# Optimization experiments

Measured on AMD Instinct MI355X. Metric: run time of the kernel, lower is better.

## Reference

```python
import jax, jax.numpy as jnp
import numpy as np

B, L, C, H, W = 2, 4, 64, 80, 80
DISCRETE_RATIO, DOWNSAMPLE_RATE, NUM_ITER = 0.4, 2, 2


def _conv2d(x, w, b):
    y = jax.lax.conv_general_dilated(x, w, (1, 1), 'SAME',
                                     dimension_numbers=('NCHW', 'OIHW', 'NCHW'))
    return y + b[None, :, None, None]


def _get_transformation_matrix(M, h, w):
    # shift(center) @ [R 0; 0 1] @ shift(-center), then add raw translation (kornia-style)
    R = M[:, :2, :2]
    center = jnp.array([w / 2.0, h / 2.0], M.dtype)
    trans = center[None, :] - jnp.einsum('nij,j->ni', R, center) + M[:, :, 2]
    return jnp.concatenate([R, trans[:, :, None]], axis=2)  # (N,2,3)


def _warp_affine(src, M, mode):
    # src (N,C,h,w); M (N,2,3) maps src pixels -> dst pixels; sample src at M^{-1} @ dst
    # (equivalent to F.affine_grid/grid_sample with align_corners=True, zeros padding)
    N, Cc, h, w = src.shape
    bottom = jnp.tile(jnp.array([[[0.0, 0.0, 1.0]]], src.dtype), (N, 1, 1))
    Minv = jnp.linalg.inv(jnp.concatenate([M, bottom], axis=1))
    yy, xx = jnp.meshgrid(jnp.arange(h, dtype=src.dtype),
                          jnp.arange(w, dtype=src.dtype), indexing='ij')
    pts = jnp.stack([xx.ravel(), yy.ravel(), jnp.ones(h * w, src.dtype)], 0)  # (3,P)
    sp = jnp.einsum('nij,jp->nip', Minv, pts)
    sx, sy = sp[:, 0], sp[:, 1]  # (N,P) source pixel coords
    flat = src.reshape(N, Cc, h * w)

    def gather(ix, iy):
        valid = ((ix >= 0) & (ix < w) & (iy >= 0) & (iy < h)).astype(src.dtype)
        idx = jnp.clip(iy, 0, h - 1) * w + jnp.clip(ix, 0, w - 1)
        vals = jnp.take_along_axis(flat, jnp.broadcast_to(idx[:, None, :], (N, Cc, h * w)), axis=2)
        return vals * valid[:, None, :]

    if mode == 'nearest':
        out = gather(jnp.round(sx).astype(jnp.int32), jnp.round(sy).astype(jnp.int32))
    else:
        x0 = jnp.floor(sx); y0 = jnp.floor(sy)
        fx = (sx - x0)[:, None, :]; fy = (sy - y0)[:, None, :]
        x0 = x0.astype(jnp.int32); y0 = y0.astype(jnp.int32)
        out = (gather(x0, y0) * (1 - fx) * (1 - fy)
               + gather(x0 + 1, y0) * fx * (1 - fy)
               + gather(x0, y0 + 1) * (1 - fx) * fy
               + gather(x0 + 1, y0 + 1) * fx * fy)
    return out.reshape(N, Cc, h, w)


def _forward(x, pairwise_t_matrix, msg_w, msg_b, gates_w, gates_b, can_w, can_b, mlp_w, mlp_b):
    feats = x.reshape(B, L, C, H, W)
    # rows [0,1], cols [0,1,3] of the 4x4 SE(3) matrices; discretize translation
    t = pairwise_t_matrix[..., :2, :][..., jnp.array([0, 1, 3])]  # (B,L,L,2,3)
    t = t.at[..., 2].set(t[..., 2] / (DISCRETE_RATIO * DOWNSAMPLE_RATE))
    T = _get_transformation_matrix(t.reshape(-1, 2, 3), H, W)  # (B*L*L,2,3), flat index (b, j, i)
    mask = _warp_affine(jnp.ones((B * L * L, 1, H, W), x.dtype), T, 'nearest').reshape(B, L, L, 1, H, W)

    for _ in range(NUM_ITER):
        # 'b c h w -> b c w h' + flip(last): coordinate-convention fix (H==W)
        y = jnp.flip(jnp.swapaxes(feats, -1, -2), axis=-1)  # (B,L,C,H,W)
        # warp neighbor j into ego i frame with T[b,j,i]
        src = jnp.broadcast_to(y[:, :, None], (B, L, L, C, H, W)).reshape(-1, C, H, W)
        neighbor = _warp_affine(src, T, 'bilinear')
        ego = jnp.broadcast_to(y[:, None], (B, L, L, C, H, W)).reshape(-1, C, H, W)
        msg = _conv2d(jnp.concatenate([neighbor, ego], axis=1), msg_w, msg_b)
        msg = msg.reshape(B, L, L, C, H, W) * mask
        agg = msg.mean(axis=1)  # 'avg' over neighbors j -> (B,L,C,H,W)
        cat_feat = jnp.concatenate([y, agg], axis=2).reshape(B * L, 2 * C, H, W)
        # single ConvGRU step with zero initial hidden state
        h0 = jnp.zeros((B * L, C, H, W), x.dtype)
        gates = _conv2d(jnp.concatenate([cat_feat, h0], axis=1), gates_w, gates_b)
        reset = jax.nn.sigmoid(gates[:, :C])
        update = jax.nn.sigmoid(gates[:, C:])
        cand = jnp.tanh(_conv2d(jnp.concatenate([cat_feat, reset * h0], axis=1), can_w, can_b))
        h1 = (1.0 - update) * h0 + update * cand
        # undo the coordinate fix: flip(last) then 'c w h -> c h w'
        feats = jnp.swapaxes(jnp.flip(h1.reshape(B, L, C, H, W), axis=-1), -1, -2)

    out = feats[:, 0]  # ego agent of each sample, (B,C,H,W)
    return jnp.einsum('bchw,oc->bhwo', out, mlp_w) + mlp_b  # nn.Linear on channel-last


def setup_inputs() -> dict:
    key = jax.random.key(0)
    ks = jax.random.split(key, 12)
    x = jax.random.normal(ks[0], (B * L, C, H, W), dtype=jnp.float32)
    record_len = jnp.full((B,), L, dtype=jnp.int32)
    # realistic SE(2) pairwise transforms embedded in 4x4 homogeneous matrices
    ang = jax.random.uniform(ks[1], (B, L, L), minval=-0.3, maxval=0.3)
    tx = jax.random.uniform(ks[2], (B, L, L), minval=-8.0, maxval=8.0)
    ty = jax.random.uniform(ks[3], (B, L, L), minval=-8.0, maxval=8.0)
    c, s = jnp.cos(ang), jnp.sin(ang)
    z, o = jnp.zeros_like(ang), jnp.ones_like(ang)
    pairwise_t_matrix = jnp.stack([c, -s, z, tx,
                                   s, c, z, ty,
                                   z, z, o, z,
                                   z, z, z, o], axis=-1).reshape(B, L, L, 4, 4).astype(jnp.float32)
    prior_encoding = jax.random.normal(ks[4], (B * L, 3), dtype=jnp.float32)  # unused by forward
    sc = 0.05
    return {
        'x': x,
        'record_len': record_len,
        'pairwise_t_matrix': pairwise_t_matrix,
        'prior_encoding': prior_encoding,
        'msg_w': jax.random.normal(ks[5], (C, 2 * C, 3, 3), dtype=jnp.float32) * sc,
        'msg_b': jnp.zeros((C,), jnp.float32),
        'gates_w': jax.random.normal(ks[6], (2 * C, 3 * C, 3, 3), dtype=jnp.float32) * sc,
        'gates_b': jnp.zeros((2 * C,), jnp.float32),
        'can_w': jax.random.normal(ks[7], (C, 3 * C, 3, 3), dtype=jnp.float32) * sc,
        'can_b': jnp.zeros((C,), jnp.float32),
        'mlp_w': jax.random.normal(ks[8], (C, C), dtype=jnp.float32) * sc,
        'mlp_b': jnp.zeros((C,), jnp.float32),
    }


def reference(x, record_len, pairwise_t_matrix, prior_encoding,
              msg_w, msg_b, gates_w, gates_b, can_w, can_b, mlp_w, mlp_b):
    # record_len is fixed to L for every sample; prior_encoding is unused by the torch forward
    return _forward(x, pairwise_t_matrix, msg_w, msg_b, gates_w, gates_b,
                    can_w, can_b, mlp_w, mlp_b)
```

## Files before the change

kernel.cpp:

```cpp
#include <hip/hip_runtime.h>
#include <math.h>

#define WD 80
#define HW 6400
#define PW 82
#define PPX 6790
#define NIMG 8
#define NPAIR 32
#define RR 4
#define STG 960

typedef short bf16x8 __attribute__((ext_vector_type(8)));
typedef float f32x4 __attribute__((ext_vector_type(4)));

__device__ __forceinline__ float bf2f(unsigned short u) {
    return __uint_as_float(((unsigned)u) << 16);
}
__device__ __forceinline__ unsigned short f2bf(float f) {
    unsigned u = __float_as_uint(f);
    u += 0x7fff + ((u >> 16) & 1);
    return (unsigned short)(u >> 16);
}

__global__ void prep_mats(const float* __restrict__ P, float* __restrict__ mats) {
    int p = threadIdx.x;
    if (p >= NPAIR) return;
    const float* m = P + p * 16;
    float m00 = m[0], m01 = m[1], m02 = m[3] / 0.8f;
    float m10 = m[4], m11 = m[5], m12 = m[7] / 0.8f;
    float cx = 40.0f, cy = 40.0f;
    float tx = cx - (m00 * cx + m01 * cy) + m02;
    float ty = cy - (m10 * cx + m11 * cy) + m12;
    float det = m00 * m11 - m01 * m10;
    float id = 1.0f / det;
    float a00 =  m11 * id, a01 = -m01 * id;
    float a10 = -m10 * id, a11 =  m00 * id;
    float a02 = -(a00 * tx + a01 * ty);
    float a12 = -(a10 * tx + a11 * ty);
    float* o = mats + p * 6;
    o[0] = a00; o[1] = a01; o[2] = a02;
    o[3] = a10; o[4] = a11; o[5] = a12;
}

__global__ void make_mask(const float* __restrict__ mats, float* __restrict__ mask) {
    int p = blockIdx.x;
    const float* a = mats + p * 6;
    float a0 = a[0], a1 = a[1], a2 = a[2], a3 = a[3], a4 = a[4], a5 = a[5];
    for (int q = threadIdx.x; q < HW; q += blockDim.x) {
        float x = (float)(q % WD), y = (float)(q / WD);
        float sx = a0 * x + a1 * y + a2;
        float sy = a3 * x + a4 * y + a5;
        int ix = (int)rintf(sx), iy = (int)rintf(sy);
        mask[p * HW + q] = (ix >= 0 && ix < WD && iy >= 0 && iy < WD) ? 1.0f : 0.0f;
    }
}

__global__ void zero_u4(uint4* __restrict__ p, int n4) {
    int t = blockIdx.x * blockDim.x + threadIdx.x;
    if (t < n4) p[t] = (uint4){0, 0, 0, 0};
}

__global__ __launch_bounds__(256) void rot_init_t(const float* __restrict__ x,
                                                  unsigned short* __restrict__ Y) {
    __shared__ float T[64][81];
    int img = blockIdx.x / 80, hh = blockIdx.x % 80;
    int tid = threadIdx.x;
    for (int idx = tid; idx < 64 * 80; idx += 256) {
        int c = idx / 80, ww = idx % 80;
        T[c][ww] = x[((size_t)(img * 64 + c) * 80 + hh) * 80 + ww];
    }
    __syncthreads();
    int b = 79 - hh;
    for (int idx = tid; idx < 80 * 64; idx += 256) {
        int a = idx >> 6, ch = idx & 63;
        Y[((size_t)img * PPX + (a + 1) * PW + (b + 1)) * 64 + ch] = f2bf(T[ch][a]);
    }
}

__global__ void prep_w(const float* __restrict__ src, unsigned short* __restrict__ dst,
                       int cin_n, int co_off, int ci_off, int co_stride) {
    int t = blockIdx.x * blockDim.x + threadIdx.x;
    if (t >= 9 * 64 * cin_n) return;
    int ci = t % cin_n;
    int co = (t / cin_n) & 63;
    int tap = t / (cin_n * 64);
    dst[t] = f2bf(src[(size_t)(co_off + co) * co_stride + (ci_off + ci) * 9 + tap]);
}

__global__ void warp_pairs(const unsigned short* __restrict__ Ysrc, const float* __restrict__ mats,
                           unsigned short* __restrict__ warped, int total, int only0) {
    int idx = blockIdx.x * blockDim.x + threadIdx.x;
    if (idx >= total) return;
    int g = idx & 7;
    int pp = (idx >> 3) % 6724;
    int k = idx / (6724 * 8);
    int p = only0 ? k * 4 : k;
    int py = pp / PW, pxx = pp % PW;
    uint4 v = {0, 0, 0, 0};
    if (py >= 1 && py <= 80 && pxx >= 1 && pxx <= 80) {
        int y = py - 1, x = pxx - 1;
        const float* a = mats + p * 6;
        float sx = a[0] * x + a[1] * y + a[2];
        float sy = a[3] * x + a[4] * y + a[5];
        float fxf = floorf(sx), fyf = floorf(sy);
        float fx = sx - fxf, fy = sy - fyf;
        int ix = (int)fxf, iy = (int)fyf;
        float w00 = (1.f - fx) * (1.f - fy), w10 = fx * (1.f - fy);
        float w01 = (1.f - fx) * fy,         w11 = fx * fy;
        bool vx0 = (unsigned)ix < WD, vx1 = (unsigned)(ix + 1) < WD;
        bool vy0 = (unsigned)iy < WD, vy1 = (unsigned)(iy + 1) < WD;
        if (!(vx0 && vy0)) w00 = 0.f;
        if (!(vx1 && vy0)) w10 = 0.f;
        if (!(vx0 && vy1)) w01 = 0.f;
        if (!(vx1 && vy1)) w11 = 0.f;
        int cx0 = min(max(ix, 0), WD - 1), cx1 = min(max(ix + 1, 0), WD - 1);
        int cy0 = min(max(iy, 0), WD - 1), cy1 = min(max(iy + 1, 0), WD - 1);
        const unsigned short* src = Ysrc + (size_t)(p >> 2) * PPX * 64 + g * 8;
        uint4 c00 = *(const uint4*)(src + ((cy0 + 1) * PW + cx0 + 1) * 64);
        uint4 c10 = *(const uint4*)(src + ((cy0 + 1) * PW + cx1 + 1) * 64);
        uint4 c01 = *(const uint4*)(src + ((cy1 + 1) * PW + cx0 + 1) * 64);
        uint4 c11 = *(const uint4*)(src + ((cy1 + 1) * PW + cx1 + 1) * 64);
        const unsigned short* p00 = (const unsigned short*)&c00;
        const unsigned short* p10 = (const unsigned short*)&c10;
        const unsigned short* p01 = (const unsigned short*)&c01;
        const unsigned short* p11 = (const unsigned short*)&c11;
        unsigned short r8[8];
#pragma unroll
        for (int kk = 0; kk < 8; ++kk) {
            float vv = w00 * bf2f(p00[kk]) + w10 * bf2f(p10[kk])
                     + w01 * bf2f(p01[kk]) + w11 * bf2f(p11[kk]);
            r8[kk] = f2bf(vv);
        }
        v = *(const uint4*)r8;
    }
    *(uint4*)(warped + ((size_t)k * PPX + pp) * 64 + g * 8) = v;
}

__device__ __forceinline__ void stage_t(const unsigned short* __restrict__ src,
                                        int x0, int y0, uint4* bufbase, int tid, int nw) {
    const int lane = tid & 63;
    const int wv = tid >> 6;
    for (int c = wv; c < STG / 64; c += nw) {
        int s = c * 64 + lane;
        int q = s >> 3;
        int yl = q / 20, xl = q - yl * 20;
        int g = (s & 7) ^ (q & 7);
        const unsigned short* gp = src + ((y0 + yl) * PW + x0 + xl) * 64 + g * 8;
        __builtin_amdgcn_global_load_lds(
            (const __attribute__((address_space(1))) unsigned int*)gp,
            (__attribute__((address_space(3))) unsigned int*)(bufbase + c * 64),
            16, 0, 0);
    }
}

__device__ __forceinline__ void load_w(const unsigned short* __restrict__ W, int row,
                                       int cinstride, int cin0, int lh, bf16x8* Wf) {
#pragma unroll
    for (int ks = 0; ks < 2; ++ks)
#pragma unroll
        for (int tap = 0; tap < 9; ++tap)
            Wf[ks * 9 + tap] = *(const bf16x8*)(W + (size_t)(tap * 64 + row) * cinstride
                                                + cin0 + ks * 32 + lh * 8);
}

__device__ __forceinline__ void conv_pass(const uint4* __restrict__ buf, const bf16x8* Wf,
                                          int ll, int lh, f32x4* acc) {
#pragma unroll
    for (int ks = 0; ks < 2; ++ks) {
        int g = ks * 4 + lh;
#pragma unroll
        for (int tap = 0; tap < 9; ++tap) {
            bf16x8 B = Wf[ks * 9 + tap];
            int ty = tap / 3, tx = tap % 3;
#pragma unroll
            for (int r = 0; r < RR; ++r) {
                int q = (r + ty) * 20 + tx + ll;
                bf16x8 A = *(const bf16x8*)&buf[q * 8 + (g ^ (q & 7))];
                acc[r] = __builtin_amdgcn_mfma_f32_16x16x32_bf16(A, B, acc[r], 0, 0, 0);
            }
        }
    }
}

__global__ __launch_bounds__(256) void msg_agg(const unsigned short* __restrict__ warped,
        const unsigned short* __restrict__ Y, const float* __restrict__ mask,
        const unsigned short* __restrict__ Wn, const unsigned short* __restrict__ We,
        const float* __restrict__ bias, unsigned short* __restrict__ Gpad, int only0) {
    __shared__ uint4 lds[2 * STG];
    __shared__ float lmask[4][RR][16];
    const int tid = threadIdx.x, lane = tid & 63, wv = tid >> 6;
    const int ll = lane & 15, lh = lane >> 4;
    const int x0 = blockIdx.x * 16, y0 = blockIdx.y * RR;
    const int t = blockIdx.z;
    const int b = only0 ? t : (t >> 2), j = only0 ? 0 : (t & 3);
    const int row = wv * 16 + ll;

    int ks_[4], ps_[4];
#pragma unroll
    for (int i = 0; i < 4; ++i) {
        int k = only0 ? (b * 4 + i) : ((b * 4 + i) * 4 + j);
        ks_[i] = k; ps_[i] = only0 ? k * 4 : k;
    }
    for (int idx = tid; idx < 4 * RR * 16; idx += 256) {
        int i = idx / (RR * 16), r = (idx >> 4) % RR, px = idx & 15;
        lmask[i][r][px] = mask[(size_t)ps_[i] * HW + (y0 + r) * WD + x0 + px];
    }
    bf16x8 Wf[18];
    load_w(Wn, row, 64, 0, lh, Wf);
    stage_t(warped + (size_t)ks_[0] * PPX * 64, x0, y0, lds, tid, 4);
    __syncthreads();

    f32x4 tot[RR];
#pragma unroll
    for (int r = 0; r < RR; ++r) tot[r] = (f32x4){0.f, 0.f, 0.f, 0.f};

    for (int i = 0; i < 4; ++i) {
        if (i < 3)
            stage_t(warped + (size_t)ks_[i + 1] * PPX * 64, x0, y0, lds + ((i + 1) & 1) * STG, tid, 4);
        f32x4 acc[RR];
#pragma unroll
        for (int r = 0; r < RR; ++r) acc[r] = (f32x4){0.f, 0.f, 0.f, 0.f};
        conv_pass(lds + (i & 1) * STG, Wf, ll, lh, acc);
#pragma unroll
        for (int r = 0; r < RR; ++r)
#pragma unroll
            for (int jj = 0; jj < 4; ++jj)
                tot[r][jj] += lmask[i][r][lh * 4 + jj] * acc[r][jj];
        __syncthreads();
    }

    load_w(We, row, 64, 0, lh, Wf);
    const int img = only0 ? t * 4 : t;
    stage_t(Y + (size_t)img * PPX * 64, x0, y0, lds, tid, 4);
    __syncthreads();
    f32x4 acc[RR];
#pragma unroll
    for (int r = 0; r < RR; ++r) acc[r] = (f32x4){0.f, 0.f, 0.f, 0.f};
    conv_pass(lds, Wf, ll, lh, acc);

    float bv = bias[row];
#pragma unroll
    for (int r = 0; r < RR; ++r)
#pragma unroll
        for (int jj = 0; jj < 4; ++jj) {
            int px = lh * 4 + jj;
            float msum = lmask[0][r][px] + lmask[1][r][px] + lmask[2][r][px] + lmask[3][r][px];
            float val = 0.25f * (tot[r][jj] + msum * (acc[r][jj] + bv));
            Gpad[((size_t)t * PPX + (y0 + r + 1) * PW + (x0 + px + 1)) * 64 + row] = f2bf(val);
        }
}

__global__ __launch_bounds__(512) void gru_conv(const unsigned short* __restrict__ Ysrc,
        const unsigned short* __restrict__ Gpad,
        const unsigned short* __restrict__ Wu, const unsigned short* __restrict__ Wc,
        const float* __restrict__ bu, const float* __restrict__ bc,
        unsigned short* __restrict__ Ydst, int only0) {
    __shared__ uint4 lds[2 * STG];
    const int tid = threadIdx.x, lane = tid & 63, w8 = tid >> 6;
    const int ll = lane & 15, lh = lane >> 4;
    const int strm = w8 >> 2, cg = w8 & 3;
    const int x0 = blockIdx.x * 16, y0 = blockIdx.y * RR;
    const int t = blockIdx.z;
    const int img = only0 ? t * 4 : t;
    const int row = cg * 16 + ll;
    const unsigned short* W = strm ? Wc : Wu;

    stage_t(Ysrc + (size_t)img * PPX * 64, x0, y0, lds, tid, 8);
    stage_t(Gpad + (size_t)t * PPX * 64, x0, y0, lds + STG, tid, 8);
    bf16x8 Wf[18];
    load_w(W, row, 128, 0, lh, Wf);
    __syncthreads();

    f32x4 acc[RR];
#pragma unroll
    for (int r = 0; r < RR; ++r) acc[r] = (f32x4){0.f, 0.f, 0.f, 0.f};
    conv_pass(lds, Wf, ll, lh, acc);
    load_w(W, row, 128, 64, lh, Wf);
    conv_pass(lds + STG, Wf, ll, lh, acc);
    __syncthreads();

    float* sig = (float*)lds;
    float bv = strm ? bc[row] : bu[row];
    if (strm == 0) {
#pragma unroll
        for (int r = 0; r < RR; ++r)
#pragma unroll
            for (int jj = 0; jj < 4; ++jj) {
                float u = 1.f / (1.f + __expf(-(acc[r][jj] + bv)));
                sig[(r * 16 + lh * 4 + jj) * 64 + row] = u;
            }
    }
    __syncthreads();
    if (strm == 1) {
#pragma unroll
        for (int r = 0; r < RR; ++r)
#pragma unroll
            for (int jj = 0; jj < 4; ++jj) {
                float c = tanhf(acc[r][jj] + bv);
                float u = sig[(r * 16 + lh * 4 + jj) * 64 + row];
                Ydst[((size_t)img * PPX + (y0 + r + 1) * PW + (x0 + lh * 4 + jj + 1)) * 64 + row]
                    = f2bf(u * c);
            }
    }
}

__global__ void final_mlp(const unsigned short* __restrict__ yfin, const float* __restrict__ mw,
                          const float* __restrict__ mb, float* __restrict__ out) {
    int t = blockIdx.x * blockDim.x + threadIdx.x;
    if (t >= 2 * HW * 64) return;
    int o  = t & 63;
    int wv = (t >> 6) % WD;
    int h  = ((t >> 6) / WD) % WD;
    int b  = t / (HW * 64);
    const unsigned short* src = yfin + ((size_t)(b * 4) * PPX + (wv + 1) * PW + (80 - h)) * 64;
    float r = mb[o];
#pragma unroll 8
    for (int c = 0; c < 64; ++c) r += bf2f(src[c]) * mw[o * 64 + c];
    out[t] = r;
}

extern "C" void kernel_launch(void* const* d_in, const int* in_sizes, int n_in,
                              void* d_out, int out_size, void* d_ws, size_t ws_size,
                              hipStream_t stream) {
    const float* x       = (const float*)d_in[0];
    const float* P       = (const float*)d_in[2];
    const float* msg_w   = (const float*)d_in[4];
    const float* msg_b   = (const float*)d_in[5];
    const float* gates_w = (const float*)d_in[6];
    const float* gates_b = (const float*)d_in[7];
    const float* can_w   = (const float*)d_in[8];
    const float* can_b   = (const float*)d_in[9];
    const float* mlp_w   = (const float*)d_in[10];
    const float* mlp_b   = (const float*)d_in[11];
    float* out = (float*)d_out;

    char* wsb = (char*)d_ws;
    float* mats = (float*)wsb;
    float* mask = (float*)(wsb + 1024);
    unsigned short* Wn = (unsigned short*)(wsb + 820224);
    unsigned short* We = Wn + 36864;
    unsigned short* Wu = We + 36864;
    unsigned short* Wc = Wu + 73728;
    unsigned short* Y0 = Wc + 73728;
    unsigned short* Y1 = Y0 + (size_t)NIMG * PPX * 64;
    unsigned short* warped = Y1 + (size_t)NIMG * PPX * 64;
    unsigned short* Gpad = warped + (size_t)NPAIR * PPX * 64;

    prep_mats<<<1, 64, 0, stream>>>(P, mats);
    make_mask<<<NPAIR, 256, 0, stream>>>(mats, mask);
    prep_w<<<(9 * 64 * 64 + 255) / 256, 256, 0, stream>>>(msg_w, Wn, 64, 0, 0, 1152);
    prep_w<<<(9 * 64 * 64 + 255) / 256, 256, 0, stream>>>(msg_w, We, 64, 0, 64, 1152);
    prep_w<<<(9 * 64 * 128 + 255) / 256, 256, 0, stream>>>(gates_w, Wu, 128, 64, 0, 1728);
    prep_w<<<(9 * 64 * 128 + 255) / 256, 256, 0, stream>>>(can_w, Wc, 128, 0, 0, 1728);
    {
        int n4a = (int)((size_t)2 * NIMG * PPX * 64 * 2 / 16);
        int n4b = (int)((size_t)NIMG * PPX * 64 * 2 / 16);
        zero_u4<<<(n4a + 255) / 256, 256, 0, stream>>>((uint4*)Y0, n4a);
        zero_u4<<<(n4b + 255) / 256, 256, 0, stream>>>((uint4*)Gpad, n4b);
    }
    rot_init_t<<<NIMG * 80, 256, 0, stream>>>(x, Y0);

    warp_pairs<<<(32 * 6724 * 8 + 255) / 256, 256, 0, stream>>>(Y0, mats, warped, 32 * 6724 * 8, 0);
    msg_agg<<<dim3(5, 80 / RR, 8), 256, 0, stream>>>(warped, Y0, mask, Wn, We, msg_b, Gpad, 0);
    gru_conv<<<dim3(5, 80 / RR, 8), 512, 0, stream>>>(Y0, Gpad, Wu, Wc, gates_b + 64, can_b, Y1, 0);

    warp_pairs<<<(8 * 6724 * 8 + 255) / 256, 256, 0, stream>>>(Y1, mats, warped, 8 * 6724 * 8, 1);
    msg_agg<<<dim3(5, 80 / RR, 2), 256, 0, stream>>>(warped, Y1, mask, Wn, We, msg_b, Gpad, 1);
    gru_conv<<<dim3(5, 80 / RR, 2), 512, 0, stream>>>(Y1, Gpad, Wu, Wc, gates_b + 64, can_b, Y0, 1);

    final_mlp<<<(2 * HW * 64 + 255) / 256, 256, 0, stream>>>(Y0, mlp_w, mlp_b, out);
}
```

Before: 277.8 us.

## Merge prep kernels, halve conv row tile, fold GRU streams into one block

Fuses the matrix-inversion and mask kernels, merges four weight-prep launches into one, and replaces two zero-fill launches with one. Halves the rows per conv tile (RR 4→2) to double the grid size. gru_conv drops from 512 to 256 threads, with each wave computing both the update and candidate convs and applying tanh inline instead of sharing results through LDS. msg_agg prefetches the ego image during the last neighbour pass, and final_mlp uses vector loads. The aim is fewer launches and better occupancy, at the cost of more redundant halo staging and twice the serial MFMA work per gru_conv wave.

```diff
diff --git a/kernel.cpp b/kernel.cpp
--- a/kernel.cpp
+++ b/kernel.cpp
@@ -7,8 +7,8 @@
 #define PPX 6790
 #define NIMG 8
 #define NPAIR 32
-#define RR 4
-#define STG 960
+#define RR 2
+#define STG 640
 
 typedef short bf16x8 __attribute__((ext_vector_type(8)));
 typedef float f32x4 __attribute__((ext_vector_type(4)));
@@ -22,34 +22,30 @@
     return (unsigned short)(u >> 16);
 }
 
-__global__ void prep_mats(const float* __restrict__ P, float* __restrict__ mats) {
-    int p = threadIdx.x;
-    if (p >= NPAIR) return;
+__device__ __forceinline__ void inv_affine(const float* __restrict__ P, int p, float* a) {
     const float* m = P + p * 16;
     float m00 = m[0], m01 = m[1], m02 = m[3] / 0.8f;
     float m10 = m[4], m11 = m[5], m12 = m[7] / 0.8f;
     float cx = 40.0f, cy = 40.0f;
     float tx = cx - (m00 * cx + m01 * cy) + m02;
     float ty = cy - (m10 * cx + m11 * cy) + m12;
-    float det = m00 * m11 - m01 * m10;
-    float id = 1.0f / det;
-    float a00 =  m11 * id, a01 = -m01 * id;
-    float a10 = -m10 * id, a11 =  m00 * id;
-    float a02 = -(a00 * tx + a01 * ty);
-    float a12 = -(a10 * tx + a11 * ty);
-    float* o = mats + p * 6;
-    o[0] = a00; o[1] = a01; o[2] = a02;
-    o[3] = a10; o[4] = a11; o[5] = a12;
-}
-
-__global__ void make_mask(const float* __restrict__ mats, float* __restrict__ mask) {
+    float id = 1.0f / (m00 * m11 - m01 * m10);
+    a[0] =  m11 * id; a[1] = -m01 * id;
+    a[3] = -m10 * id; a[4] =  m00 * id;
+    a[2] = -(a[0] * tx + a[1] * ty);
+    a[5] = -(a[3] * tx + a[4] * ty);
+}
+
+__global__ void make_mask2(const float* __restrict__ P, float* __restrict__ mats,
+                           float* __restrict__ mask) {
     int p = blockIdx.x;
-    const float* a = mats + p * 6;
-    float a0 = a[0], a1 = a[1], a2 = a[2], a3 = a[3], a4 = a[4], a5 = a[5];
+    float a[6];
+    inv_affine(P, p, a);
+    if (threadIdx.x < 6) mats[p * 6 + threadIdx.x] = a[threadIdx.x];
     for (int q = threadIdx.x; q < HW; q += blockDim.x) {
         float x = (float)(q % WD), y = (float)(q / WD);
-        float sx = a0 * x + a1 * y + a2;
-        float sy = a3 * x + a4 * y + a5;
+        float sx = a[0] * x + a[1] * y + a[2];
+        float sy = a[3] * x + a[4] * y + a[5];
         int ix = (int)rintf(sx), iy = (int)rintf(sy);
         mask[p * HW + q] = (ix >= 0 && ix < WD && iy >= 0 && iy < WD) ? 1.0f : 0.0f;
     }
@@ -77,14 +73,22 @@
     }
 }
 
-__global__ void prep_w(const float* __restrict__ src, unsigned short* __restrict__ dst,
-                       int cin_n, int co_off, int ci_off, int co_stride) {
+__global__ void prep_w_all(const float* __restrict__ msg_w, const float* __restrict__ gates_w,
+                           const float* __restrict__ can_w,
+                           unsigned short* __restrict__ Wn, unsigned short* __restrict__ We,
+                           unsigned short* __restrict__ Wu, unsigned short* __restrict__ Wc) {
     int t = blockIdx.x * blockDim.x + threadIdx.x;
-    if (t >= 9 * 64 * cin_n) return;
-    int ci = t % cin_n;
-    int co = (t / cin_n) & 63;
-    int tap = t / (cin_n * 64);
-    dst[t] = f2bf(src[(size_t)(co_off + co) * co_stride + (ci_off + ci) * 9 + tap]);
+    if (t >= 221184) return;
+    const float* src; unsigned short* dst;
+    int cin_n, co_off, ci_off, stride, u;
+    if (t < 36864)       { src = msg_w;   dst = Wn; cin_n = 64;  co_off = 0;  ci_off = 0;  stride = 1152; u = t; }
+    else if (t < 73728)  { src = msg_w;   dst = We; cin_n = 64;  co_off = 0;  ci_off = 64; stride = 1152; u = t - 36864; }
+    else if (t < 147456) { src = gates_w; dst = Wu; cin_n = 128; co_off = 64; ci_off = 0;  stride = 1728; u = t - 73728; }
+    else                 { src = can_w;   dst = Wc; cin_n = 128; co_off = 0;  ci_off = 0;  stride = 1728; u = t - 147456; }
+    int ci = u % cin_n;
+    int co = (u / cin_n) & 63;
+    int tap = u / (cin_n * 64);
+    dst[u] = f2bf(src[(size_t)(co_off + co) * stride + (ci_off + ci) * 9 + tap]);
 }
 
 __global__ void warp_pairs(const unsigned short* __restrict__ Ysrc, const float* __restrict__ mats,
@@ -137,10 +141,10 @@
 }
 
 __device__ __forceinline__ void stage_t(const unsigned short* __restrict__ src,
-                                        int x0, int y0, uint4* bufbase, int tid, int nw) {
+                                        int x0, int y0, uint4* bufbase, int tid) {
     const int lane = tid & 63;
     const int wv = tid >> 6;
-    for (int c = wv; c < STG / 64; c += nw) {
+    for (int c = wv; c < STG / 64; c += 4) {
         int s = c * 64 + lane;
         int q = s >> 3;
         int yl = q / 20, xl = q - yl * 20;
@@ -194,20 +198,20 @@
     const int t = blockIdx.z;
     const int b = only0 ? t : (t >> 2), j = only0 ? 0 : (t & 3);
     const int row = wv * 16 + ll;
-
-    int ks_[4], ps_[4];
-#pragma unroll
-    for (int i = 0; i < 4; ++i) {
-        int k = only0 ? (b * 4 + i) : ((b * 4 + i) * 4 + j);
-        ks_[i] = k; ps_[i] = only0 ? k * 4 : k;
-    }
-    for (int idx = tid; idx < 4 * RR * 16; idx += 256) {
-        int i = idx / (RR * 16), r = (idx >> 4) % RR, px = idx & 15;
-        lmask[i][r][px] = mask[(size_t)ps_[i] * HW + (y0 + r) * WD + x0 + px];
+    const int img = only0 ? t * 4 : t;
+
+    int ks_[4];
+#pragma unroll
+    for (int i = 0; i < 4; ++i)
+        ks_[i] = only0 ? (b * 4 + i) : ((b * 4 + i) * 4 + j);
+    if (tid < 4 * RR * 16) {
+        int i = tid / (RR * 16), r = (tid >> 4) % RR, px = tid & 15;
+        int p = only0 ? ks_[i] * 4 : ks_[i];
+        lmask[i][r][px] = mask[(size_t)p * HW + (y0 + r) * WD + x0 + px];
     }
     bf16x8 Wf[18];
     load_w(Wn, row, 64, 0, lh, Wf);
-    stage_t(warped + (size_t)ks_[0] * PPX * 64, x0, y0, lds, tid, 4);
+    stage_t(warped + (size_t)ks_[0] * PPX * 64, x0, y0, lds, tid);
     __syncthreads();
 
     f32x4 tot[RR];
@@ -216,7 +220,9 @@
 
     for (int i = 0; i < 4; ++i) {
         if (i < 3)
-            stage_t(warped + (size_t)ks_[i + 1] * PPX * 64, x0, y0, lds + ((i + 1) & 1) * STG, tid, 4);
+            stage_t(warped + (size_t)ks_[i + 1] * PPX * 64, x0, y0, lds + ((i + 1) & 1) * STG, tid);
+        else
+            stage_t(Y + (size_t)img * PPX * 64, x0, y0, lds, tid);
         f32x4 acc[RR];
 #pragma unroll
         for (int r = 0; r < RR; ++r) acc[r] = (f32x4){0.f, 0.f, 0.f, 0.f};
@@ -230,9 +236,6 @@
     }
 
     load_w(We, row, 64, 0, lh, Wf);
-    const int img = only0 ? t * 4 : t;
-    stage_t(Y + (size_t)img * PPX * 64, x0, y0, lds, tid, 4);
-    __syncthreads();
     f32x4 acc[RR];
 #pragma unroll
     for (int r = 0; r < RR; ++r) acc[r] = (f32x4){0.f, 0.f, 0.f, 0.f};
@@ -250,58 +253,50 @@
         }
 }
 
-__global__ __launch_bounds__(512) void gru_conv(const unsigned short* __restrict__ Ysrc,
+__global__ __launch_bounds__(256) void gru_conv(const unsigned short* __restrict__ Ysrc,
         const unsigned short* __restrict__ Gpad,
         const unsigned short* __restrict__ Wu, const unsigned short* __restrict__ Wc,
         const float* __restrict__ bu, const float* __restrict__ bc,
         unsigned short* __restrict__ Ydst, int only0) {
     __shared__ uint4 lds[2 * STG];
-    const int tid = threadIdx.x, lane = tid & 63, w8 = tid >> 6;
+    const int tid = threadIdx.x, lane = tid & 63, wv = tid >> 6;
     const int ll = lane & 15, lh = lane >> 4;
-    const int strm = w8 >> 2, cg = w8 & 3;
     const int x0 = blockIdx.x * 16, y0 = blockIdx.y * RR;
     const int t = blockIdx.z;
     const int img = only0 ? t * 4 : t;
-    const int row = cg * 16 + ll;
-    const unsigned short* W = strm ? Wc : Wu;
-
-    stage_t(Ysrc + (size_t)img * PPX * 64, x0, y0, lds, tid, 8);
-    stage_t(Gpad + (size_t)t * PPX * 64, x0, y0, lds + STG, tid, 8);
+    const int row = wv * 16 + ll;
+
+    stage_t(Ysrc + (size_t)img * PPX * 64, x0, y0, lds, tid);
+    stage_t(Gpad + (size_t)t * PPX * 64, x0, y0, lds + STG, tid);
     bf16x8 Wf[18];
-    load_w(W, row, 128, 0, lh, Wf);
+    load_w(Wu, row, 128, 0, lh, Wf);
     __syncthreads();
 
-    f32x4 acc[RR];
-#pragma unroll
-    for (int r = 0; r < RR; ++r) acc[r] = (f32x4){0.f, 0.f, 0.f, 0.f};
-    conv_pass(lds, Wf, ll, lh, acc);
-    load_w(W, row, 128, 64, lh, Wf);
-    conv_pass(lds + STG, Wf, ll, lh, acc);
-    __syncthreads();
-
-    float* sig = (float*)lds;
-    float bv = strm ? bc[row] : bu[row];
-    if (strm == 0) {
-#pragma unroll
-        for (int r = 0; r < RR; ++r)
-#pragma unroll
-            for (int jj = 0; jj < 4; ++jj) {
-                float u = 1.f / (1.f + __expf(-(acc[r][jj] + bv)));
-                sig[(r * 16 + lh * 4 + jj) * 64 + row] = u;
-            }
-    }
-    __syncthreads();
-    if (strm == 1) {
-#pragma unroll
-        for (int r = 0; r < RR; ++r)
-#pragma unroll
-            for (int jj = 0; jj < 4; ++jj) {
-                float c = tanhf(acc[r][jj] + bv);
-                float u = sig[(r * 16 + lh * 4 + jj) * 64 + row];
-                Ydst[((size_t)img * PPX + (y0 + r + 1) * PW + (x0 + lh * 4 + jj + 1)) * 64 + row]
-                    = f2bf(u * c);
-            }
-    }
+    f32x4 aU[RR], aC[RR];
+#pragma unroll
+    for (int r = 0; r < RR; ++r) {
+        aU[r] = (f32x4){0.f, 0.f, 0.f, 0.f};
+        aC[r] = (f32x4){0.f, 0.f, 0.f, 0.f};
+    }
+    conv_pass(lds, Wf, ll, lh, aU);
+    load_w(Wu, row, 128, 64, lh, Wf);
+    conv_pass(lds + STG, Wf, ll, lh, aU);
+    load_w(Wc, row, 128, 0, lh, Wf);
+    conv_pass(lds, Wf, ll, lh, aC);
+    load_w(Wc, row, 128, 64, lh, Wf);
+    conv_pass(lds + STG, Wf, ll, lh, aC);
+
+    float ub = bu[row], cb = bc[row];
+#pragma unroll
+    for (int r = 0; r < RR; ++r)
+#pragma unroll
+        for (int jj = 0; jj < 4; ++jj) {
+            float u = 1.f / (1.f + __expf(-(aU[r][jj] + ub)));
+            float e2 = __expf(2.f * (aC[r][jj] + cb));
+            float c = (e2 - 1.f) / (e2 + 1.f);
+            Ydst[((size_t)img * PPX + (y0 + r + 1) * PW + (x0 + lh * 4 + jj + 1)) * 64 + row]
+                = f2bf(u * c);
+        }
 }
 
 __global__ void final_mlp(const unsigned short* __restrict__ yfin, const float* __restrict__ mw,
@@ -313,9 +308,15 @@
     int h  = ((t >> 6) / WD) % WD;
     int b  = t / (HW * 64);
     const unsigned short* src = yfin + ((size_t)(b * 4) * PPX + (wv + 1) * PW + (80 - h)) * 64;
+    const float* wrow = mw + o * 64;
     float r = mb[o];
-#pragma unroll 8
-    for (int c = 0; c < 64; ++c) r += bf2f(src[c]) * mw[o * 64 + c];
+#pragma unroll
+    for (int c8 = 0; c8 < 8; ++c8) {
+        bf16x8 v = *(const bf16x8*)(src + c8 * 8);
+#pragma unroll
+        for (int k = 0; k < 8; ++k)
+            r += bf2f(((const unsigned short*)&v)[k]) * wrow[c8 * 8 + k];
+    }
     out[t] = r;
 }
 
@@ -343,30 +344,24 @@
     unsigned short* Wc = Wu + 73728;
     unsigned short* Y0 = Wc + 73728;
     unsigned short* Y1 = Y0 + (size_t)NIMG * PPX * 64;
-    unsigned short* warped = Y1 + (size_t)NIMG * PPX * 64;
-    unsigned short* Gpad = warped + (size_t)NPAIR * PPX * 64;
-
-    prep_mats<<<1, 64, 0, stream>>>(P, mats);
-    make_mask<<<NPAIR, 256, 0, stream>>>(mats, mask);
-    prep_w<<<(9 * 64 * 64 + 255) / 256, 256, 0, stream>>>(msg_w, Wn, 64, 0, 0, 1152);
-    prep_w<<<(9 * 64 * 64 + 255) / 256, 256, 0, stream>>>(msg_w, We, 64, 0, 64, 1152);
-    prep_w<<<(9 * 64 * 128 + 255) / 256, 256, 0, stream>>>(gates_w, Wu, 128, 64, 0, 1728);
-    prep_w<<<(9 * 64 * 128 + 255) / 256, 256, 0, stream>>>(can_w, Wc, 128, 0, 0, 1728);
+    unsigned short* Gpad = Y1 + (size_t)NIMG * PPX * 64;
+    unsigned short* warped = Gpad + (size_t)NIMG * PPX * 64;
+
     {
-        int n4a = (int)((size_t)2 * NIMG * PPX * 64 * 2 / 16);
-        int n4b = (int)((size_t)NIMG * PPX * 64 * 2 / 16);
-        zero_u4<<<(n4a + 255) / 256, 256, 0, stream>>>((uint4*)Y0, n4a);
-        zero_u4<<<(n4b + 255) / 256, 256, 0, stream>>>((uint4*)Gpad, n4b);
-    }
+        int n4 = (int)((size_t)3 * NIMG * PPX * 64 * 2 / 16);
+        zero_u4<<<(n4 + 255) / 256, 256, 0, stream>>>((uint4*)Y0, n4);
+    }
+    make_mask2<<<NPAIR, 256, 0, stream>>>(P, mats, mask);
+    prep_w_all<<<(221184 + 255) / 256, 256, 0, stream>>>(msg_w, gates_w, can_w, Wn, We, Wu, Wc);
     rot_init_t<<<NIMG * 80, 256, 0, stream>>>(x, Y0);
 
     warp_pairs<<<(32 * 6724 * 8 + 255) / 256, 256, 0, stream>>>(Y0, mats, warped, 32 * 6724 * 8, 0);
     msg_agg<<<dim3(5, 80 / RR, 8), 256, 0, stream>>>(warped, Y0, mask, Wn, We, msg_b, Gpad, 0);
-    gru_conv<<<dim3(5, 80 / RR, 8), 512, 0, stream>>>(Y0, Gpad, Wu, Wc, gates_b + 64, can_b, Y1, 0);
+    gru_conv<<<dim3(5, 80 / RR, 8), 256, 0, stream>>>(Y0, Gpad, Wu, Wc, gates_b + 64, can_b, Y1, 0);
 
     warp_pairs<<<(8 * 6724 * 8 + 255) / 256, 256, 0, stream>>>(Y1, mats, warped, 8 * 6724 * 8, 1);
     msg_agg<<<dim3(5, 80 / RR, 2), 256, 0, stream>>>(warped, Y1, mask, Wn, We, msg_b, Gpad, 1);
-    gru_conv<<<dim3(5, 80 / RR, 2), 512, 0, stream>>>(Y1, Gpad, Wu, Wc, gates_b + 64, can_b, Y0, 1);
+    gru_conv<<<dim3(5, 80 / RR, 2), 256, 0, stream>>>(Y1, Gpad, Wu, Wc, gates_b + 64, can_b, Y0, 1);
 
     final_mlp<<<(2 * HW * 64 + 255) / 256, 256, 0, stream>>>(Y0, mlp_w, mlp_b, out);
 }
```

Result: no change. 282.6 us (+1.7%).
